# Performance work log

Hardware: AMD Instinct MI355X
Metric: run time of the kernel (lower is better)

The kernel has to match this reference:

```python
import jax, jax.numpy as jnp
import numpy as np


def setup_inputs() -> dict:
    key = jax.random.key(0)
    k1, k2, k3, k4 = jax.random.split(key, 4)
    c = 256
    x = jax.random.normal(k1, (4, c, 64, 64), dtype=jnp.float32)
    # 1x1 conv weights act as channel-mixing matrices
    w_qkv = jax.random.normal(k2, (3 * c, c), dtype=jnp.float32) * (1.0 / np.sqrt(c))
    w_out = jax.random.normal(k3, (c, c), dtype=jnp.float32) * (1.0 / np.sqrt(c))
    b_out = jax.random.normal(k4, (c,), dtype=jnp.float32) * 0.01
    return {"x": x, "w_qkv": w_qkv, "w_out": w_out, "b_out": b_out}


def reference(x, w_qkv, w_out, b_out):
    b, c, h, w = x.shape
    heads = 4
    d = c // heads
    scale = d ** (-0.5)
    hw = h * w

    # 1x1 conv (no bias): [b,3c,h,w]
    qkv = jnp.einsum('oc,bchw->bohw', w_qkv, x)
    q, k, v = jnp.split(qkv, 3, axis=1)

    def to_seq(t):
        # [b,c,h,w] -> [b,heads,hw,d]
        return t.reshape(b, heads, d, hw).transpose(0, 1, 3, 2)

    q, k, v = to_seq(q), to_seq(k), to_seq(v)

    sim = jnp.einsum('bhid,bhjd->bhij', q, k) * scale
    attn = jax.nn.softmax(sim, axis=-1)
    out = jnp.einsum('bhij,bhjd->bhid', attn, v)

    # [b,heads,hw,d] -> [b,c,h,w]
    out = out.transpose(0, 1, 3, 2).reshape(b, c, h, w)

    # output 1x1 conv with bias, plus residual
    proj = jnp.einsum('oc,bchw->bohw', w_out, out) + b_out[None, :, None, None]
    return x + proj
```

## Files before the change

### kernel.cpp

```cpp
#include <hip/hip_runtime.h>


#define HW 4096
#define CIN 256
#define LOG2E_DIV8 0.18033688011112042f

typedef __attribute__((ext_vector_type(8))) short short8v;
typedef __attribute__((ext_vector_type(4))) short short4v;
typedef __attribute__((ext_vector_type(4))) float float4v;
typedef __attribute__((ext_vector_type(16))) float f32x16;
typedef __attribute__((ext_vector_type(4))) unsigned int uint4v;

static __device__ __forceinline__ unsigned short f2bf(float f) {
    unsigned int u = __float_as_uint(f);
    u += 0x7fff + ((u >> 16) & 1);
    return (unsigned short)(u >> 16);
}
static __device__ __forceinline__ unsigned int pkbf(float a, float b) {
    unsigned int r;
    asm("v_cvt_pk_bf16_f32 %0, %1, %2" : "=v"(r) : "v"(a), "v"(b));
    return r;
}
static __device__ __forceinline__ void pl32swap(unsigned int& a, unsigned int& b) {
    asm volatile("v_permlane32_swap_b32 %0, %1" : "+v"(a), "+v"(b));
}

__global__ __launch_bounds__(256) void cast_w_k(
    const float* __restrict__ w_qkv, const float* __restrict__ w_out,
    unsigned short* __restrict__ wqb, unsigned short* __restrict__ wob)
{
    const int bi = blockIdx.x;
    if (bi < 192) {
        const int idx = bi * 1024 + threadIdx.x * 4;
        const float s = (idx < 256 * 256) ? LOG2E_DIV8 : 1.0f;
        const float4 v = *(const float4*)&w_qkv[idx];
        uint2 pk;
        pk.x = pkbf(v.x * s, v.y * s);
        pk.y = pkbf(v.z * s, v.w * s);
        *(uint2*)&wqb[idx] = pk;
    } else {
        const int idx = (bi - 192) * 1024 + threadIdx.x * 4;
        const float4 v = *(const float4*)&w_out[idx];
        uint2 pk;
        pk.x = pkbf(v.x, v.y);
        pk.y = pkbf(v.z, v.w);
        *(uint2*)&wob[idx] = pk;
    }
}

__global__ __launch_bounds__(256) void cast_x_k(
    const float* __restrict__ x, unsigned short* __restrict__ xt)
{
    const int p0 = blockIdx.x * 64, c0 = blockIdx.y * 64, b = blockIdx.z;
    const int t = threadIdx.x;
    __shared__ float tile[64][65];

    const float* xb = x + ((size_t)b * CIN + c0) * HW + p0;
    #pragma unroll
    for (int iter = 0; iter < 4; ++iter) {
        const int idx = iter * 1024 + t * 4;
        const int cc = idx >> 6, pp = idx & 63;
        const float4 v = *(const float4*)&xb[(size_t)cc * HW + pp];
        tile[cc][pp + 0] = v.x; tile[cc][pp + 1] = v.y;
        tile[cc][pp + 2] = v.z; tile[cc][pp + 3] = v.w;
    }
    __syncthreads();
    unsigned short* xo = xt + ((size_t)b * HW + p0) * CIN + c0;
    #pragma unroll
    for (int iter = 0; iter < 4; ++iter) {
        const int idx = iter * 1024 + t * 4;
        const int pp = idx >> 6, cc = idx & 63;
        uint2 pk;
        pk.x = pkbf(tile[cc + 0][pp], tile[cc + 1][pp]);
        pk.y = pkbf(tile[cc + 2][pp], tile[cc + 3][pp]);
        *(uint2*)&xo[(size_t)pp * CIN + cc] = pk;
    }
}

__global__ __launch_bounds__(256) void qkv_mfma_k(
    const unsigned short* __restrict__ wqb, const unsigned short* __restrict__ xt,
    unsigned short* __restrict__ qb, unsigned short* __restrict__ kb,
    unsigned short* __restrict__ vb)
{
    const int o0 = blockIdx.x * 128;
    const int p0 = blockIdx.y * 128;
    const int b  = blockIdx.z;
    const int t = threadIdx.x;
    const int wid = t >> 6, lane = t & 63, g = lane >> 4, li = lane & 15;
    const int wo = (wid >> 1) * 64, wp = (wid & 1) * 64;

    __shared__ char alds[16384];
    __shared__ char blds[16384];

    const int srow8 = t >> 3, sc16 = t & 7;
    const char* asrc = (const char*)wqb + ((size_t)(o0 + srow8) * 256) * 2 + sc16 * 16;
    const char* bsrc = (const char*)xt + (((size_t)b * HW + p0 + srow8) * 256) * 2 + sc16 * 16;

    float4 areg[4], breg[4];
    #pragma unroll
    for (int it = 0; it < 4; ++it) {
        areg[it] = *(const float4*)(asrc + (size_t)it * 32 * 512);
        breg[it] = *(const float4*)(bsrc + (size_t)it * 32 * 512);
    }

    float4v acc[4][4];
    #pragma unroll
    for (int mt = 0; mt < 4; ++mt)
        #pragma unroll
        for (int nt = 0; nt < 4; ++nt) acc[mt][nt] = (float4v){0.f, 0.f, 0.f, 0.f};

    for (int ks = 0; ks < 4; ++ks) {
        #pragma unroll
        for (int it = 0; it < 4; ++it) {
            const int row = it * 32 + srow8;
            const int dsw = row * 128 + ((sc16 * 16) ^ ((row & 7) << 4));
            *(float4*)(alds + dsw) = areg[it];
            *(float4*)(blds + dsw) = breg[it];
        }
        __syncthreads();
        if (ks < 3) {
            #pragma unroll
            for (int it = 0; it < 4; ++it) {
                areg[it] = *(const float4*)(asrc + (size_t)it * 32 * 512 + (ks + 1) * 128);
                breg[it] = *(const float4*)(bsrc + (size_t)it * 32 * 512 + (ks + 1) * 128);
            }
        }
        short8v af[4][2], bf[4][2];
        #pragma unroll
        for (int mt = 0; mt < 4; ++mt) {
            const int row = wo + mt * 16 + li;
            #pragma unroll
            for (int kc = 0; kc < 2; ++kc)
                af[mt][kc] = *(const short8v*)(alds + row * 128 + ((kc * 64 + g * 16) ^ ((row & 7) << 4)));
        }
        #pragma unroll
        for (int nt = 0; nt < 4; ++nt) {
            const int row = wp + nt * 16 + li;
            #pragma unroll
            for (int kc = 0; kc < 2; ++kc)
                bf[nt][kc] = *(const short8v*)(blds + row * 128 + ((kc * 64 + g * 16) ^ ((row & 7) << 4)));
        }
        #pragma unroll
        for (int mt = 0; mt < 4; ++mt)
            #pragma unroll
            for (int nt = 0; nt < 4; ++nt) {
                acc[mt][nt] = __builtin_amdgcn_mfma_f32_16x16x32_bf16(af[mt][0], bf[nt][0], acc[mt][nt], 0, 0, 0);
                acc[mt][nt] = __builtin_amdgcn_mfma_f32_16x16x32_bf16(af[mt][1], bf[nt][1], acc[mt][nt], 0, 0, 0);
            }
        __syncthreads();
    }

    const int which = o0 >> 8;
    #pragma unroll
    for (int mt = 0; mt < 4; ++mt) {
        const int o_b = o0 + wo + mt * 16 + g * 4;
        const int head = (o_b >> 6) & 3;
        const int dd = o_b & 63;
        const int bh = b * 4 + head;
        if (which < 2) {
            unsigned short* dst = which ? kb : qb;
            #pragma unroll
            for (int nt = 0; nt < 4; ++nt) {
                const int p = p0 + wp + nt * 16 + li;
                uint2 pk;
                pk.x = pkbf(acc[mt][nt][0], acc[mt][nt][1]);
                pk.y = pkbf(acc[mt][nt][2], acc[mt][nt][3]);
                *(uint2*)&dst[((size_t)bh * HW + p) * 64 + dd] = pk;
            }
        } else {
            #pragma unroll
            for (int nt = 0; nt < 4; ++nt) {
                const int p = p0 + wp + nt * 16 + li;
                #pragma unroll
                for (int r = 0; r < 4; ++r)
                    vb[((size_t)bh * 64 + dd + r) * HW + p] = f2bf(acc[mt][nt][r]);
            }
        }
    }
}

__global__ __launch_bounds__(256) void flash_mfma_k(
    const unsigned short* __restrict__ qb, const unsigned short* __restrict__ kb,
    const unsigned short* __restrict__ vb, unsigned short* __restrict__ att)
{
    const int i0 = blockIdx.x * 128;
    const int bh = blockIdx.y;
    const int t = threadIdx.x;
    const int wid = t >> 6, lane = t & 63;
    const int q32 = lane & 31, hi = lane >> 5;
    const int b = bh >> 2, head = bh & 3;

    const unsigned short* qg = qb + (size_t)bh * HW * 64;
    const unsigned short* kg = kb + (size_t)bh * HW * 64;
    const unsigned short* vg = vb + (size_t)bh * 64 * HW;

    __shared__ char klds[2][8192];
    __shared__ char vlds[2][8192];

    const int q = i0 + wid * 32 + q32;
    short8v qf[4];
    #pragma unroll
    for (int kc = 0; kc < 4; ++kc)
        qf[kc] = *(const short8v*)(qg + (size_t)q * 64 + kc * 16 + hi * 8);

    short8v ones;
    #pragma unroll
    for (int i = 0; i < 8; ++i) ones[i] = (short)0x3F80;

    float m = 0.f;
    f32x16 acco[2];
    f32x16 accl;
    f32x16 accs[2];
    short8v pf[2][2];
    #pragma unroll
    for (int r = 0; r < 16; ++r) { acco[0][r] = 0.f; acco[1][r] = 0.f; accl[r] = 0.f; }

    const int srow0 = t >> 3, sc0 = t & 7;
    const int srow1 = srow0 + 32;
    const int dsw0 = srow0 * 128 + ((sc0 * 16) ^ ((srow0 & 7) << 4));
    const int dsw1 = srow1 * 128 + ((sc0 * 16) ^ ((srow1 & 7) << 4));
    const char* ksrc0 = (const char*)kg + (size_t)srow0 * 128 + sc0 * 16;
    const char* ksrc1 = (const char*)kg + (size_t)srow1 * 128 + sc0 * 16;
    const char* vsrc0 = (const char*)vg + (size_t)srow0 * 8192 + sc0 * 16;
    const char* vsrc1 = (const char*)vg + (size_t)srow1 * 8192 + sc0 * 16;

    float4 kregA, kregB, vregA, vregB;

    auto LOADT = [&](int tile) {
        kregA = *(const float4*)(ksrc0 + (size_t)tile * 8192);
        kregB = *(const float4*)(ksrc1 + (size_t)tile * 8192);
        vregA = *(const float4*)(vsrc0 + (size_t)tile * 128);
        vregB = *(const float4*)(vsrc1 + (size_t)tile * 128);
    };
    auto WRITET = [&](int buf) {
        *(float4*)(klds[buf] + dsw0) = kregA;
        *(float4*)(klds[buf] + dsw1) = kregB;
        *(float4*)(vlds[buf] + dsw0) = vregA;
        *(float4*)(vlds[buf] + dsw1) = vregB;
    };
    auto SMM = [&](int buf) {
        #pragma unroll
        for (int r = 0; r < 16; ++r) { accs[0][r] = -m; accs[1][r] = -m; }
        __builtin_amdgcn_s_setprio(1);
        #pragma unroll
        for (int jt = 0; jt < 2; ++jt) {
            const int row = jt * 32 + q32;
            const char* kbase = klds[buf] + row * 128;
            const int sw = (row & 7) << 4;
            #pragma unroll
            for (int kc = 0; kc < 4; ++kc) {
                const short8v kf = *(const short8v*)(kbase + ((kc * 32 + hi * 16) ^ sw));
                accs[jt] = __builtin_amdgcn_mfma_f32_32x32x16_bf16(kf, qf[kc], accs[jt], 0, 0, 0);
            }
        }
        __builtin_amdgcn_s_setprio(0);
    };
    auto SOFT = [&]() {
        float mx[16];
        #pragma unroll
        for (int r = 0; r < 16; ++r) mx[r] = fmaxf(accs[0][r], accs[1][r]);
        #pragma unroll
        for (int s = 8; s > 0; s >>= 1)
            #pragma unroll
            for (int r = 0; r < s; ++r) mx[r] = fmaxf(mx[r], mx[r + s]);
        const float tm = fmaxf(mx[0], __shfl_xor(mx[0], 32, 64));
        if (__any(tm > 8.0f)) {
            const float delta = fmaxf(tm, 0.f);
            const float fsc = __builtin_amdgcn_exp2f(-delta);
            m += delta;
            accl[0] *= fsc;
            #pragma unroll
            for (int r = 0; r < 16; ++r) { acco[0][r] *= fsc; acco[1][r] *= fsc; }
            #pragma unroll
            for (int r = 0; r < 16; ++r) { accs[0][r] -= delta; accs[1][r] -= delta; }
        }
        #pragma unroll
        for (int jt = 0; jt < 2; ++jt) {
            float p[16];
            #pragma unroll
            for (int r = 0; r < 16; ++r) p[r] = __builtin_amdgcn_exp2f(accs[jt][r]);
            unsigned int w0 = pkbf(p[0], p[1]);
            unsigned int w1 = pkbf(p[2], p[3]);
            unsigned int w2 = pkbf(p[4], p[5]);
            unsigned int w3 = pkbf(p[6], p[7]);
            pl32swap(w0, w2);
            pl32swap(w1, w3);
            uint4v fa; fa[0] = w0; fa[1] = w1; fa[2] = w2; fa[3] = w3;
            pf[jt][0] = __builtin_bit_cast(short8v, fa);
            unsigned int w4 = pkbf(p[8],  p[9]);
            unsigned int w5 = pkbf(p[10], p[11]);
            unsigned int w6 = pkbf(p[12], p[13]);
            unsigned int w7 = pkbf(p[14], p[15]);
            pl32swap(w4, w6);
            pl32swap(w5, w7);
            uint4v fb; fb[0] = w4; fb[1] = w5; fb[2] = w6; fb[3] = w7;
            pf[jt][1] = __builtin_bit_cast(short8v, fb);
        }
    };
    auto PVMM = [&](int buf) {
        __builtin_amdgcn_s_setprio(1);
        #pragma unroll
        for (int jt = 0; jt < 2; ++jt)
            #pragma unroll
            for (int kr = 0; kr < 2; ++kr)
                accl = __builtin_amdgcn_mfma_f32_32x32x16_bf16(ones, pf[jt][kr], accl, 0, 0, 0);
        #pragma unroll
        for (int dt = 0; dt < 2; ++dt) {
            const int row = dt * 32 + q32;
            const char* vbase = vlds[buf] + row * 128;
            const int sw = (row & 7) << 4;
            #pragma unroll
            for (int jt = 0; jt < 2; ++jt)
                #pragma unroll
                for (int kr = 0; kr < 2; ++kr) {
                    const short8v vf = *(const short8v*)(vbase + ((jt * 64 + kr * 32 + hi * 16) ^ sw));
                    acco[dt] = __builtin_amdgcn_mfma_f32_32x32x16_bf16(vf, pf[jt][kr], acco[dt], 0, 0, 0);
                }
        }
        __builtin_amdgcn_s_setprio(0);
    };

    LOADT(0);
    WRITET(0);
    LOADT(1);
    __syncthreads();
    SMM(0);

    for (int kt = 0; kt < 63; ++kt) {
        const int nb = (kt + 1) & 1;
        WRITET(nb);
        const int pref = (kt + 2 < 64) ? kt + 2 : 63;
        LOADT(pref);
        SOFT();
        PVMM(kt & 1);
        __syncthreads();
        SMM(nb);
    }
    SOFT();
    PVMM(1);

    const float inv = 1.0f / accl[0];
    unsigned short* ao = att + ((size_t)b * HW + q) * CIN + head * 64;
    #pragma unroll
    for (int dt = 0; dt < 2; ++dt)
        #pragma unroll
        for (int g4 = 0; g4 < 4; ++g4) {
            const int d = dt * 32 + 8 * g4 + 4 * hi;
            uint2 pk;
            pk.x = pkbf(acco[dt][g4 * 4 + 0] * inv, acco[dt][g4 * 4 + 1] * inv);
            pk.y = pkbf(acco[dt][g4 * 4 + 2] * inv, acco[dt][g4 * 4 + 3] * inv);
            *(uint2*)&ao[d] = pk;
        }
}

__global__ __launch_bounds__(256) void proj_mfma_k(
    const unsigned short* __restrict__ wob, const unsigned short* __restrict__ att,
    const float* __restrict__ bias, const float* __restrict__ x,
    float* __restrict__ out)
{
    const int o0 = blockIdx.x * 128;
    const int p0 = blockIdx.y * 128;
    const int b  = blockIdx.z;
    const int t = threadIdx.x;
    const int wid = t >> 6, lane = t & 63, g = lane >> 4, li = lane & 15;
    const int wo = (wid >> 1) * 64, wp = (wid & 1) * 64;

    __shared__ char alds[16384];
    __shared__ char blds[16384];

    const int srow8 = t >> 3, sc16 = t & 7;
    const char* asrc = (const char*)wob + ((size_t)(o0 + srow8) * 256) * 2 + sc16 * 16;
    const char* bsrc = (const char*)att + (((size_t)b * HW + p0 + srow8) * 256) * 2 + sc16 * 16;

    float4 areg[4], breg[4];
    #pragma unroll
    for (int it = 0; it < 4; ++it) {
        areg[it] = *(const float4*)(asrc + (size_t)it * 32 * 512);
        breg[it] = *(const float4*)(bsrc + (size_t)it * 32 * 512);
    }

    float4v acc[4][4];
    #pragma unroll
    for (int mt = 0; mt < 4; ++mt)
        #pragma unroll
        for (int nt = 0; nt < 4; ++nt) acc[mt][nt] = (float4v){0.f, 0.f, 0.f, 0.f};

    for (int ks = 0; ks < 4; ++ks) {
        #pragma unroll
        for (int it = 0; it < 4; ++it) {
            const int row = it * 32 + srow8;
            const int dsw = row * 128 + ((sc16 * 16) ^ ((row & 7) << 4));
            *(float4*)(alds + dsw) = areg[it];
            *(float4*)(blds + dsw) = breg[it];
        }
        __syncthreads();
        if (ks < 3) {
            #pragma unroll
            for (int it = 0; it < 4; ++it) {
                areg[it] = *(const float4*)(asrc + (size_t)it * 32 * 512 + (ks + 1) * 128);
                breg[it] = *(const float4*)(bsrc + (size_t)it * 32 * 512 + (ks + 1) * 128);
            }
        }
        short8v af[4][2], bf[4][2];
        #pragma unroll
        for (int mt = 0; mt < 4; ++mt) {
            const int row = wo + mt * 16 + li;
            #pragma unroll
            for (int kc = 0; kc < 2; ++kc)
                af[mt][kc] = *(const short8v*)(alds + row * 128 + ((kc * 64 + g * 16) ^ ((row & 7) << 4)));
        }
        #pragma unroll
        for (int nt = 0; nt < 4; ++nt) {
            const int row = wp + nt * 16 + li;
            #pragma unroll
            for (int kc = 0; kc < 2; ++kc)
                bf[nt][kc] = *(const short8v*)(blds + row * 128 + ((kc * 64 + g * 16) ^ ((row & 7) << 4)));
        }
        #pragma unroll
        for (int mt = 0; mt < 4; ++mt)
            #pragma unroll
            for (int nt = 0; nt < 4; ++nt) {
                acc[mt][nt] = __builtin_amdgcn_mfma_f32_16x16x32_bf16(af[mt][0], bf[nt][0], acc[mt][nt], 0, 0, 0);
                acc[mt][nt] = __builtin_amdgcn_mfma_f32_16x16x32_bf16(af[mt][1], bf[nt][1], acc[mt][nt], 0, 0, 0);
            }
        __syncthreads();
    }

    #pragma unroll
    for (int mt = 0; mt < 4; ++mt) {
        const int o_b = o0 + wo + mt * 16 + g * 4;
        #pragma unroll
        for (int nt = 0; nt < 4; ++nt) {
            const int p = p0 + wp + nt * 16 + li;
            #pragma unroll
            for (int r = 0; r < 4; ++r) {
                const int o = o_b + r;
                const size_t ix = ((size_t)b * CIN + o) * HW + p;
                out[ix] = acc[mt][nt][r] + bias[o] + x[ix];
            }
        }
    }
}

extern "C" void kernel_launch(void* const* d_in, const int* in_sizes, int n_in,
                              void* d_out, int out_size, void* d_ws, size_t ws_size,
                              hipStream_t stream)
{
    const float* x     = (const float*)d_in[0];
    const float* w_qkv = (const float*)d_in[1];
    const float* w_out = (const float*)d_in[2];
    const float* b_out = (const float*)d_in[3];
    float* out = (float*)d_out;

    char* ws = (char*)d_ws;
    const size_t MB = 1024 * 1024;
    unsigned short* xt  = (unsigned short*)(ws);
    unsigned short* qb  = (unsigned short*)(ws + 8 * MB);
    unsigned short* kb  = (unsigned short*)(ws + 16 * MB);
    unsigned short* vb  = (unsigned short*)(ws + 24 * MB);
    unsigned short* att = (unsigned short*)(ws + 32 * MB);
    unsigned short* wqb = (unsigned short*)(ws + 40 * MB);
    unsigned short* wob = (unsigned short*)(ws + 40 * MB + 768 * 256 * 2);

    cast_w_k<<<256, 256, 0, stream>>>(w_qkv, w_out, wqb, wob);
    cast_x_k<<<dim3(64, 4, 4), 256, 0, stream>>>(x, xt);
    qkv_mfma_k<<<dim3(6, 32, 4), 256, 0, stream>>>(wqb, xt, qb, kb, vb);
    flash_mfma_k<<<dim3(32, 16), 256, 0, stream>>>(qb, kb, vb, att);
    proj_mfma_k<<<dim3(2, 32, 4), 256, 0, stream>>>(wob, att, b_out, x, out);
}
```

Baseline: 162.7 us.

## Split flash attention key range across two wave groups and merge via LDS

Flash kernel now launches 512 threads per block: two groups of four waves each process half of the key/value sequence for the same 128 queries, then combine partial outputs, maxima and sums through shared memory. This raises the number of active waves per CU, since the grid was only 512 blocks of 4 waves, so more memory and MFMA latency can be hidden. The cost is 64KB of LDS per block, an extra merge step with a barrier, and half the waves sitting idle during the final write. The row-max reduction is also reshaped into three-input max chains.

Result: slower. 272.9 us (+67.8%).

```diff
diff --git a/kernel.cpp b/kernel.cpp
--- a/kernel.cpp
+++ b/kernel.cpp
@@ -23,6 +23,9 @@
 }
 static __device__ __forceinline__ void pl32swap(unsigned int& a, unsigned int& b) {
     asm volatile("v_permlane32_swap_b32 %0, %1" : "+v"(a), "+v"(b));
+}
+static __device__ __forceinline__ float fmax3(float a, float b, float c) {
+    return fmaxf(fmaxf(a, b), c);
 }
 
 __global__ __launch_bounds__(256) void cast_w_k(
@@ -179,7 +182,7 @@
     }
 }
 
-__global__ __launch_bounds__(256) void flash_mfma_k(
+__global__ __launch_bounds__(512, 4) void flash_mfma_k(
     const unsigned short* __restrict__ qb, const unsigned short* __restrict__ kb,
     const unsigned short* __restrict__ vb, unsigned short* __restrict__ att)
 {
@@ -188,16 +191,19 @@
     const int t = threadIdx.x;
     const int wid = t >> 6, lane = t & 63;
     const int q32 = lane & 31, hi = lane >> 5;
+    const int sp = t >> 8;
+    const int w4 = wid & 3;
     const int b = bh >> 2, head = bh & 3;
 
     const unsigned short* qg = qb + (size_t)bh * HW * 64;
-    const unsigned short* kg = kb + (size_t)bh * HW * 64;
-    const unsigned short* vg = vb + (size_t)bh * 64 * HW;
-
-    __shared__ char klds[2][8192];
-    __shared__ char vlds[2][8192];
-
-    const int q = i0 + wid * 32 + q32;
+    const unsigned short* kg = kb + (size_t)bh * HW * 64 + (size_t)sp * 2048 * 64;
+    const unsigned short* vg = vb + (size_t)bh * 64 * HW + (size_t)sp * 2048;
+
+    __shared__ char smem[65536];
+    char* const kls = smem + sp * 16384;
+    char* const vls = smem + 32768 + sp * 16384;
+
+    const int q = i0 + w4 * 32 + q32;
     short8v qf[4];
     #pragma unroll
     for (int kc = 0; kc < 4; ++kc)
@@ -215,7 +221,8 @@
     #pragma unroll
     for (int r = 0; r < 16; ++r) { acco[0][r] = 0.f; acco[1][r] = 0.f; accl[r] = 0.f; }
 
-    const int srow0 = t >> 3, sc0 = t & 7;
+    const int ts = t & 255;
+    const int srow0 = ts >> 3, sc0 = ts & 7;
     const int srow1 = srow0 + 32;
     const int dsw0 = srow0 * 128 + ((sc0 * 16) ^ ((srow0 & 7) << 4));
     const int dsw1 = srow1 * 128 + ((sc0 * 16) ^ ((srow1 & 7) << 4));
@@ -233,10 +240,10 @@
         vregB = *(const float4*)(vsrc1 + (size_t)tile * 128);
     };
     auto WRITET = [&](int buf) {
-        *(float4*)(klds[buf] + dsw0) = kregA;
-        *(float4*)(klds[buf] + dsw1) = kregB;
-        *(float4*)(vlds[buf] + dsw0) = vregA;
-        *(float4*)(vlds[buf] + dsw1) = vregB;
+        *(float4*)(kls + buf * 8192 + dsw0) = kregA;
+        *(float4*)(kls + buf * 8192 + dsw1) = kregB;
+        *(float4*)(vls + buf * 8192 + dsw0) = vregA;
+        *(float4*)(vls + buf * 8192 + dsw1) = vregB;
     };
     auto SMM = [&](int buf) {
         #pragma unroll
@@ -245,7 +252,7 @@
         #pragma unroll
         for (int jt = 0; jt < 2; ++jt) {
             const int row = jt * 32 + q32;
-            const char* kbase = klds[buf] + row * 128;
+            const char* kbase = kls + buf * 8192 + row * 128;
             const int sw = (row & 7) << 4;
             #pragma unroll
             for (int kc = 0; kc < 4; ++kc) {
@@ -259,11 +266,15 @@
         float mx[16];
         #pragma unroll
         for (int r = 0; r < 16; ++r) mx[r] = fmaxf(accs[0][r], accs[1][r]);
-        #pragma unroll
-        for (int s = 8; s > 0; s >>= 1)
-            #pragma unroll
-            for (int r = 0; r < s; ++r) mx[r] = fmaxf(mx[r], mx[r + s]);
-        const float tm = fmaxf(mx[0], __shfl_xor(mx[0], 32, 64));
+        float a0 = fmax3(mx[0],  mx[1],  mx[2]);
+        float a1 = fmax3(mx[3],  mx[4],  mx[5]);
+        float a2 = fmax3(mx[6],  mx[7],  mx[8]);
+        float a3 = fmax3(mx[9],  mx[10], mx[11]);
+        float a4 = fmax3(mx[12], mx[13], mx[14]);
+        float b0 = fmax3(a0, a1, a2);
+        float b1 = fmax3(a3, a4, mx[15]);
+        float tm = fmaxf(b0, b1);
+        tm = fmaxf(tm, __shfl_xor(tm, 32, 64));
         if (__any(tm > 8.0f)) {
             const float delta = fmaxf(tm, 0.f);
             const float fsc = __builtin_amdgcn_exp2f(-delta);
@@ -287,13 +298,13 @@
             pl32swap(w1, w3);
             uint4v fa; fa[0] = w0; fa[1] = w1; fa[2] = w2; fa[3] = w3;
             pf[jt][0] = __builtin_bit_cast(short8v, fa);
-            unsigned int w4 = pkbf(p[8],  p[9]);
+            unsigned int w4_ = pkbf(p[8],  p[9]);
             unsigned int w5 = pkbf(p[10], p[11]);
             unsigned int w6 = pkbf(p[12], p[13]);
             unsigned int w7 = pkbf(p[14], p[15]);
-            pl32swap(w4, w6);
+            pl32swap(w4_, w6);
             pl32swap(w5, w7);
-            uint4v fb; fb[0] = w4; fb[1] = w5; fb[2] = w6; fb[3] = w7;
+            uint4v fb; fb[0] = w4_; fb[1] = w5; fb[2] = w6; fb[3] = w7;
             pf[jt][1] = __builtin_bit_cast(short8v, fb);
         }
     };
@@ -307,7 +318,7 @@
         #pragma unroll
         for (int dt = 0; dt < 2; ++dt) {
             const int row = dt * 32 + q32;
-            const char* vbase = vlds[buf] + row * 128;
+            const char* vbase = vls + buf * 8192 + row * 128;
             const int sw = (row & 7) << 4;
             #pragma unroll
             for (int jt = 0; jt < 2; ++jt)
@@ -326,10 +337,10 @@
     __syncthreads();
     SMM(0);
 
-    for (int kt = 0; kt < 63; ++kt) {
+    for (int kt = 0; kt < 31; ++kt) {
         const int nb = (kt + 1) & 1;
         WRITET(nb);
-        const int pref = (kt + 2 < 64) ? kt + 2 : 63;
+        const int pref = (kt + 2 < 32) ? kt + 2 : 31;
         LOADT(pref);
         SOFT();
         PVMM(kt & 1);
@@ -339,18 +350,48 @@
     SOFT();
     PVMM(1);
 
-    const float inv = 1.0f / accl[0];
-    unsigned short* ao = att + ((size_t)b * HW + q) * CIN + head * 64;
-    #pragma unroll
-    for (int dt = 0; dt < 2; ++dt)
-        #pragma unroll
-        for (int g4 = 0; g4 < 4; ++g4) {
-            const int d = dt * 32 + 8 * g4 + 4 * hi;
-            uint2 pk;
-            pk.x = pkbf(acco[dt][g4 * 4 + 0] * inv, acco[dt][g4 * 4 + 1] * inv);
-            pk.y = pkbf(acco[dt][g4 * 4 + 2] * inv, acco[dt][g4 * 4 + 3] * inv);
-            *(uint2*)&ao[d] = pk;
-        }
+    __syncthreads();
+    float* ex  = (float*)smem;
+    float* mlx = (float*)(smem + 32768);
+    if (sp == 1) {
+        #pragma unroll
+        for (int dt = 0; dt < 2; ++dt)
+            #pragma unroll
+            for (int r = 0; r < 16; ++r) {
+                const int d = dt * 32 + 8 * (r >> 2) + 4 * hi + (r & 3);
+                ex[w4 * 2048 + d * 32 + q32] = acco[dt][r];
+            }
+        if (hi == 0) {
+            mlx[(w4 * 32 + q32) * 2 + 0] = m;
+            mlx[(w4 * 32 + q32) * 2 + 1] = accl[0];
+        }
+    }
+    __syncthreads();
+    if (sp == 0) {
+        const float m1 = mlx[(w4 * 32 + q32) * 2 + 0];
+        const float l1 = mlx[(w4 * 32 + q32) * 2 + 1];
+        const float mxm = fmaxf(m, m1);
+        float f0 = __builtin_amdgcn_exp2f(m - mxm);
+        float f1 = __builtin_amdgcn_exp2f(m1 - mxm);
+        const float inv = 1.0f / (accl[0] * f0 + l1 * f1);
+        f0 *= inv; f1 *= inv;
+        unsigned short* ao = att + ((size_t)b * HW + q) * CIN + head * 64;
+        #pragma unroll
+        for (int dt = 0; dt < 2; ++dt)
+            #pragma unroll
+            for (int g4 = 0; g4 < 4; ++g4) {
+                const int d0 = dt * 32 + 8 * g4 + 4 * hi;
+                const float* exb = ex + w4 * 2048 + d0 * 32 + q32;
+                const float v0 = acco[dt][g4 * 4 + 0] * f0 + exb[0]  * f1;
+                const float v1 = acco[dt][g4 * 4 + 1] * f0 + exb[32] * f1;
+                const float v2 = acco[dt][g4 * 4 + 2] * f0 + exb[64] * f1;
+                const float v3 = acco[dt][g4 * 4 + 3] * f0 + exb[96] * f1;
+                uint2 pk;
+                pk.x = pkbf(v0, v1);
+                pk.y = pkbf(v2, v3);
+                *(uint2*)&ao[d0] = pk;
+            }
+    }
 }
 
 __global__ __launch_bounds__(256) void proj_mfma_k(
@@ -465,6 +506,6 @@
     cast_w_k<<<256, 256, 0, stream>>>(w_qkv, w_out, wqb, wob);
     cast_x_k<<<dim3(64, 4, 4), 256, 0, stream>>>(x, xt);
     qkv_mfma_k<<<dim3(6, 32, 4), 256, 0, stream>>>(wqb, xt, qb, kb, vb);
-    flash_mfma_k<<<dim3(32, 16), 256, 0, stream>>>(qb, kb, vb, att);
+    flash_mfma_k<<<dim3(32, 16), 512, 0, stream>>>(qb, kb, vb, att);
     proj_mfma_k<<<dim3(2, 32, 4), 256, 0, stream>>>(wob, att, b_out, x, out);
 }
```
